# Performance work log

Hardware: AMD Instinct MI355X
Metric: run time of the kernel (lower is better)

Reference implementation:

```python
import jax, jax.numpy as jnp
import numpy as np

BS, L, D = 64, 100, 512
ITEM_NUM = 100000
N = BS * (L + 1)  # number of in-batch candidate items
MASK_VAL = -10000.0


def setup_inputs() -> dict:
    key = jax.random.key(0)
    ks = jax.random.split(key, 8)
    sample_items_id = jax.random.randint(ks[0], (BS, L + 1), 1, ITEM_NUM + 1, dtype=jnp.int32)
    log_mask = jax.random.randint(ks[1], (BS, L), 0, 2, dtype=jnp.int32)
    pop_prob = jax.random.uniform(ks[2], (ITEM_NUM + 1,), minval=1e-3, maxval=1.0, dtype=jnp.float32)
    id_emb = jax.random.normal(ks[3], (ITEM_NUM + 1, D), dtype=jnp.float32) * 0.02
    scale = 1.0 / np.sqrt(D)
    W_ih = jax.random.normal(ks[4], (D, 3 * D), dtype=jnp.float32) * scale
    W_hh = jax.random.normal(ks[5], (D, 3 * D), dtype=jnp.float32) * scale
    b_ih = jnp.zeros((3 * D,), jnp.float32)
    b_hh = jnp.zeros((3 * D,), jnp.float32)
    return dict(sample_items_id=sample_items_id, log_mask=log_mask, pop_prob=pop_prob,
                id_emb=id_emb, W_ih=W_ih, W_hh=W_hh, b_ih=b_ih, b_hh=b_hh)


def gru_forward(x, W_ih, W_hh, b_ih, b_hh):
    # x: (B, T, D) -> per-step hidden states (B, T, D)  (GRU4Rec user encoder)
    B, T, Dh = x.shape
    gates_x = jnp.einsum('btd,de->bte', x, W_ih) + b_ih  # precompute input gates (B,T,3D)

    def step(h, gx):
        gh = h @ W_hh + b_hh
        xr, xz, xn = jnp.split(gx, 3, axis=-1)
        hr, hz, hn = jnp.split(gh, 3, axis=-1)
        r = jax.nn.sigmoid(xr + hr)
        z = jax.nn.sigmoid(xz + hz)
        n = jnp.tanh(xn + r * hn)
        h_new = (1.0 - z) * n + z * h
        return h_new, h_new

    h0 = jnp.zeros((B, Dh), x.dtype)
    _, hs = jax.lax.scan(step, h0, jnp.swapaxes(gates_x, 0, 1))  # (T,B,D)
    return jnp.swapaxes(hs, 0, 1)


def reference(sample_items_id, log_mask, pop_prob, id_emb, W_ih, W_hh, b_ih, b_hh):
    ids_flat = sample_items_id.reshape(-1)                 # (N,)
    debias = jnp.log(pop_prob[ids_flat])                   # (N,) debias_logits
    score_embs = id_emb[ids_flat]                          # (N, D)
    input_embs = score_embs.reshape(BS, L + 1, D)
    prec = gru_forward(input_embs[:, :-1, :], W_ih, W_hh, b_ih, b_hh)  # (BS, L, D)
    prec_vec = prec.reshape(BS * L, D)

    logits = prec_vec @ score_embs.T - debias[None, :]     # (BS*L, N)
    # mask padded candidate columns: cat(log_mask, ones(bs,1)) flattened == 0
    col_valid = jnp.concatenate([log_mask, jnp.ones((BS, 1), log_mask.dtype)], axis=1).reshape(-1)
    logits = jnp.where(col_valid[None, :] == 0, MASK_VAL, logits)
    logits = logits.reshape(BS, L, N)

    # per-sample negative exclusion: column k is rejected for sample i if
    # ids_flat[k] appears anywhere in sample i's own item list
    reject = (ids_flat[None, None, :] == sample_items_id[:, :, None]).any(axis=1)  # (BS, N)
    mask3 = jnp.broadcast_to(reject[:, None, :], (BS, L, N))
    # keep the ground-truth target position (i, j, i*(L+1)+j+1) unmasked
    tgt = jnp.arange(BS)[:, None] * (L + 1) + jnp.arange(L)[None, :] + 1  # (BS, L)
    col = jnp.arange(N)[None, None, :]
    mask3 = mask3 & (col != tgt[:, :, None])
    logits = jnp.where(mask3, MASK_VAL, logits)

    logits = logits.reshape(BS * L, N)
    labels = tgt.reshape(-1)
    logp = jax.nn.log_softmax(logits, axis=-1)
    nll = -jnp.take_along_axis(logp, labels[:, None], axis=1)[:, 0]
    w = (log_mask.reshape(-1) != 0).astype(logits.dtype)
    loss = jnp.sum(nll * w) / jnp.maximum(jnp.sum(w), 1.0)
    return loss
```

## Files before the change

kernel.cpp:

```cpp
#include <hip/hip_runtime.h>
#include <hip/hip_bf16.h>

#define BSZ   64
#define SEQL  100
#define DIM   512
#define L1P   101
#define NCOLS 6464
#define NROWS 6400
#define D3    1536
#define MASKV -10000.0f
#define M0    16.0f

#define SGRP  4
#define SPG   16
#define DBLK  16
#define DPB   32
#define GRU_BLOCKS (SGRP * DBLK)
#define SENT64 0x7FC07FC07FC07FC0ULL
#define INIT_N  409600
#define INIT_NP 410624

typedef __attribute__((ext_vector_type(8))) short bf16x8;
typedef __attribute__((ext_vector_type(4))) float f32x4;

__device__ __forceinline__ float sigm(float x)  { return 1.f / (1.f + __expf(-x)); }
__device__ __forceinline__ float ftanh(float x) { float e = __expf(2.f * x); return 1.f - 2.f / (e + 1.f); }
__device__ __forceinline__ ushort f2bf(float x) {
    __hip_bfloat16 b = __float2bfloat16(x);
    return *(ushort*)&b;
}

__global__ void init_ws(float* s_glob, float* acc, uint4* prec_all)
{
    int t = blockIdx.x * 256 + threadIdx.x;
    if (t < INIT_N) {
        uint4 s; s.x = 0x7FC07FC0u; s.y = 0x7FC07FC0u; s.z = 0x7FC07FC0u; s.w = 0x7FC07FC0u;
        prec_all[t] = s;
    } else if (t < INIT_NP) {
        uint4 z; z.x = 0u; z.y = 0u; z.z = 0u; z.w = 0u;
        prec_all[t] = z;
    }
    if (t < NROWS) s_glob[t] = 0.f;
    if (t < 2) acc[t] = 0.f;
}

__global__ void gather_embs(const int* __restrict__ ids, const float* __restrict__ emb,
                            ushort* __restrict__ score16)
{
    int idx = blockIdx.x * 256 + threadIdx.x;
    int row = idx >> 7, c4 = idx & 127;
    int id = ids[row];
    float4 v = *(const float4*)&emb[(size_t)id * DIM + c4 * 4];
    ushort4 u;
    u.x = f2bf(v.x); u.y = f2bf(v.y); u.z = f2bf(v.z); u.w = f2bf(v.w);
    *(ushort4*)&score16[(size_t)row * DIM + c4 * 4] = u;
}

__global__ void aux_kernel(const int* __restrict__ ids, const float* __restrict__ pop,
                           const int* __restrict__ lmask,
                           float* __restrict__ debias, int* __restrict__ colv)
{
    int k = blockIdx.x * 256 + threadIdx.x;
    if (k >= NCOLS) return;
    int id = ids[k];
    debias[k] = __logf(pop[id]);
    int j = k % L1P;
    colv[k] = (j == SEQL) ? 1 : lmask[(k / L1P) * SEQL + j];
}

__global__ void build_reject(const int* __restrict__ ids, const int* __restrict__ colv,
                             unsigned char* __restrict__ rejm)
{
    __shared__ int s_ids[L1P];
    int i = blockIdx.y;
    int tid = threadIdx.x;
    if (tid < L1P) s_ids[tid] = ids[i * L1P + tid];
    __syncthreads();
    int k = blockIdx.x * 256 + tid;
    if (k >= NCOLS) return;
    int myid = ids[k];
    int rej = 0;
    for (int j = 0; j < L1P; ++j) rej |= (myid == s_ids[j]);
    unsigned char code = (colv[k] == 0) ? 1 : (rej ? 2 : 0);
    rejm[(size_t)i * NCOLS + k] = code;
}

__global__ __launch_bounds__(256) void wt_tile(const float* __restrict__ W,
                                               ushort* __restrict__ WT)
{
    __shared__ float tile[64][65];
    int c0 = blockIdx.x * 64, k0 = blockIdx.y * 64;
    int tx = threadIdx.x & 63, ty = threadIdx.x >> 6;
    for (int r = ty; r < 64; r += 4)
        tile[r][tx] = W[(size_t)(k0 + r) * D3 + c0 + tx];
    __syncthreads();
    for (int r = ty; r < 64; r += 4)
        WT[(size_t)(c0 + r) * DIM + k0 + tx] = f2bf(tile[tx][r]);
}

__global__ __launch_bounds__(256, 1) void gates_mfma(
    const ushort* __restrict__ score16, const ushort* __restrict__ WIT,
    const float* __restrict__ b_ih, float* __restrict__ gates)
{
    __shared__ ushort Bs[64 * 512];
    int n0 = blockIdx.x * 64;
    int rowbase = blockIdx.y * 640;
    int tid = threadIdx.x;
    int w = tid >> 6, lane = tid & 63, l15 = lane & 15, quad = lane >> 4;

    {
        const char* slab = (const char*)(WIT + (size_t)n0 * DIM);
#pragma unroll
        for (int k = 0; k < 16; ++k) {
            int o  = k * 4096 + w * 1024 + lane * 16;
            int so = o ^ (((o >> 10) & 15) << 4);
            __builtin_amdgcn_global_load_lds(
                (const __attribute__((address_space(1))) void*)(slab + so),
                (__attribute__((address_space(3))) void*)((char*)Bs + k * 4096 + w * 1024),
                16, 0, 0);
        }
    }
    float bi[4];
#pragma unroll
    for (int nt = 0; nt < 4; ++nt) bi[nt] = b_ih[n0 + nt * 16 + l15];

    asm volatile("s_waitcnt vmcnt(0)" ::: "memory");
    __syncthreads();

    int key = l15 << 4;
    bf16x8 afA[16], afB[16];

    auto load_af = [&](bf16x8 (&dst)[16], int rt) {
        int r = rowbase + rt * 64 + w * 16 + l15;
        int i = r / SEQL, j = r - i * SEQL;
        const ushort* ap = score16 + (size_t)(i * L1P + j) * DIM + quad * 8;
#pragma unroll
        for (int c = 0; c < 16; ++c) dst[c] = *(const bf16x8*)(ap + c * 32);
    };
    auto do_tile = [&](const bf16x8 (&af)[16], int rt) {
        f32x4 acc[4] = {{0,0,0,0},{0,0,0,0},{0,0,0,0},{0,0,0,0}};
        const char* bt = (const char*)Bs;
#pragma unroll
        for (int c = 0; c < 16; ++c) {
#pragma unroll
            for (int nt = 0; nt < 4; ++nt) {
                int a = (nt * 16 + l15) * 1024 + ((c * 64 + quad * 16) ^ key);
                bf16x8 bb = *(const bf16x8*)(bt + a);
                acc[nt] = __builtin_amdgcn_mfma_f32_16x16x32_bf16(af[c], bb, acc[nt], 0, 0, 0);
            }
        }
#pragma unroll
        for (int nt = 0; nt < 4; ++nt) {
#pragma unroll
            for (int p = 0; p < 4; ++p) {
                int rr = rowbase + rt * 64 + w * 16 + quad * 4 + p;
                gates[(size_t)rr * D3 + n0 + nt * 16 + l15] = acc[nt][p] + bi[nt];
            }
        }
    };

    load_af(afA, 0);
#pragma unroll
    for (int rp = 0; rp < 5; ++rp) {
        load_af(afB, rp * 2 + 1);
        do_tile(afA, rp * 2);
        if (rp < 4) load_af(afA, rp * 2 + 2);
        do_tile(afB, rp * 2 + 1);
    }
}

__global__ __launch_bounds__(256) void gru_mfma(
    const ushort* __restrict__ WT,
    const float* __restrict__ b_hh,
    const float* __restrict__ gates,
    ushort* __restrict__ prec16)
{
    __shared__ float red[2][2][3][256];

    int b = blockIdx.x;
    int sg = b >> 4, db = b & 15;
    int s0 = sg * SPG, d0 = db * DPB;
    int tid = threadIdx.x;
    int w = tid >> 6, lane = tid & 63, l15 = lane & 15, quad = lane >> 4;
    int wc = w & 1, wk = w >> 1;
    int kb = wk * 8;

    bf16x8 wreg[3][8];
#pragma unroll
    for (int g = 0; g < 3; ++g)
#pragma unroll
        for (int cc = 0; cc < 8; ++cc)
            wreg[g][cc] = *(const bf16x8*)(WT
                + (size_t)(g * 512 + d0 + wc * 16 + l15) * DIM
                + (kb + cc) * 32 + quad * 8);

    int d = d0 + wc * 16 + l15;
    float bhr = b_hh[d], bhz = b_hh[512 + d], bhn = b_hh[1024 + d];
    float hprev[4] = {0.f, 0.f, 0.f, 0.f};

    for (int t = 0; t < SEQL; ++t) {
        int tp = t & 1;
        float xr[4], xz[4], xn[4];
        if (wk == 0) {
#pragma unroll
            for (int p = 0; p < 4; ++p) {
                int ss = s0 + quad * 4 + p;
                const float* gx = gates + ((size_t)ss * SEQL + t) * D3;
                xr[p] = gx[d]; xz[p] = gx[512 + d]; xn[p] = gx[1024 + d];
            }
        }
        f32x4 acc[3] = {{0,0,0,0},{0,0,0,0},{0,0,0,0}};
        if (t > 0) {
            const ushort* ap = prec16
                + ((size_t)(s0 + l15) * SEQL + (t - 1)) * DIM + quad * 8;
            unsigned long long v[16];
            bool again = true;
            while (again) {
#pragma unroll
                for (int u = 0; u < 16; ++u) {
                    const unsigned long long* p64 = (const unsigned long long*)
                        (ap + (kb + (u >> 1)) * 32 + (u & 1) * 4);
                    v[u] = __hip_atomic_load(p64, __ATOMIC_RELAXED,
                                             __HIP_MEMORY_SCOPE_AGENT);
                }
                unsigned long long bad = 0ull;
#pragma unroll
                for (int u = 0; u < 16; ++u) {
                    unsigned long long x = v[u] ^ SENT64;
                    bad |= (x - 0x0001000100010001ULL) & ~x & 0x8000800080008000ULL;
                }
                again = (bad != 0ull);
                if (again) __builtin_amdgcn_s_sleep(1);
            }
#pragma unroll
            for (int cc = 0; cc < 8; ++cc) {
                union { unsigned long long q[2]; bf16x8 h; } af;
                af.q[0] = v[2 * cc]; af.q[1] = v[2 * cc + 1];
#pragma unroll
                for (int g = 0; g < 3; ++g)
                    acc[g] = __builtin_amdgcn_mfma_f32_16x16x32_bf16(
                        af.h, wreg[g][cc], acc[g], 0, 0, 0);
            }
        }
        if (wk == 1) {
#pragma unroll
            for (int g = 0; g < 3; ++g)
                *(f32x4*)&red[tp][wc][g][lane * 4] = acc[g];
        }
        __syncthreads();
        if (wk == 0) {
#pragma unroll
            for (int p = 0; p < 4; ++p) {
                float a0 = acc[0][p] + red[tp][wc][0][lane * 4 + p];
                float a1 = acc[1][p] + red[tp][wc][1][lane * 4 + p];
                float a2 = acc[2][p] + red[tp][wc][2][lane * 4 + p];
                float r = sigm(xr[p] + a0 + bhr);
                float z = sigm(xz[p] + a1 + bhz);
                float n = ftanh(xn[p] + r * (a2 + bhn));
                float hnew = (1.f - z) * n + z * hprev[p];
                hprev[p] = hnew;
                unsigned b16 = f2bf(hnew);
                unsigned lo = b16 | (((unsigned)__shfl_xor((int)b16, 1)) << 16);
                unsigned long long hi = (unsigned)__shfl_xor((int)lo, 2);
                unsigned long long vv = (unsigned long long)lo | (hi << 32);
                if ((l15 & 3) == 0) {
                    unsigned long long* dst = (unsigned long long*)
                        (prec16 + ((size_t)(s0 + quad * 4 + p) * SEQL + t) * DIM
                         + d0 + wc * 16 + l15);
                    __hip_atomic_store(dst, vv, __ATOMIC_RELAXED,
                                       __HIP_MEMORY_SCOPE_AGENT);
                }
            }
        }
    }
}

__global__ __launch_bounds__(256, 2) void logits_mfma(
    const ushort* __restrict__ prec16, const ushort* __restrict__ score16,
    const float* __restrict__ debias, const unsigned char* __restrict__ rejm,
    float* __restrict__ s_glob, float* __restrict__ label_glob)
{
    __shared__ ushort Bt[2][16 * 512];
    __shared__ float dbs[816];
    __shared__ unsigned char rjs[816];

    int bi = blockIdx.x;
    int i  = bi >> 3;
    int cs = (bi >> 1) & 3;
    int h  = bi & 1;
    int tile0  = cs * 101 + h * 51;
    int ntiles = 51 - h;
    int tid  = threadIdx.x;
    int lane = tid & 63;
    int w    = tid >> 6;
    int l15  = lane & 15, quad = lane >> 4;

    bf16x8 afrag[2][16];
    bool live1 = (w < 3);
    {
        int r0 = i * SEQL + (2 * w) * 16 + l15;
        const ushort* ap = prec16 + (size_t)r0 * DIM + quad * 8;
#pragma unroll
        for (int c = 0; c < 16; ++c) afrag[0][c] = *(const bf16x8*)(ap + c * 32);
    }
    if (live1) {
        int r1 = i * SEQL + (2 * w + 1) * 16 + l15;
        const ushort* ap = prec16 + (size_t)r1 * DIM + quad * 8;
#pragma unroll
        for (int c = 0; c < 16; ++c) afrag[1][c] = *(const bf16x8*)(ap + c * 32);
    }

    int ncols = ntiles * 16;
    int nb0 = tile0 * 16;
    for (int idx = tid; idx < ncols; idx += 256) {
        dbs[idx] = debias[nb0 + idx];
        rjs[idx] = rejm[(size_t)i * NCOLS + nb0 + idx];
    }

    auto stage = [&](int buf, int st) {
        const char* slab = (const char*)(score16 + (size_t)(tile0 + st) * 16 * DIM);
#pragma unroll
        for (int k = 0; k < 4; ++k) {
            int o  = k * 4096 + w * 1024 + lane * 16;
            int so = o ^ (((o >> 10) & 15) << 4);
            __builtin_amdgcn_global_load_lds(
                (const __attribute__((address_space(1))) void*)(slab + so),
                (__attribute__((address_space(3))) void*)((char*)&Bt[buf][0] + k * 4096 + w * 1024),
                16, 0, 0);
        }
    };

    stage(0, 0);
    asm volatile("s_waitcnt vmcnt(0)" ::: "memory");
    __syncthreads();

    float srun0[4] = {0.f, 0.f, 0.f, 0.f};
    float srun1[4] = {0.f, 0.f, 0.f, 0.f};
    int colb = l15 * 1024;
    int q16  = quad * 16;
    int key  = l15 << 4;

    for (int st = 0; st < ntiles; ++st) {
        int cur = st & 1;
        if (st + 1 < ntiles) stage(cur ^ 1, st + 1);

        const char* bt = (const char*)&Bt[cur][0];
        f32x4 acc0[2] = {{0,0,0,0},{0,0,0,0}};
        f32x4 acc1[2] = {{0,0,0,0},{0,0,0,0}};
#pragma unroll
        for (int c = 0; c < 16; ++c) {
            int a = colb + ((c * 64 + q16) ^ key);
            bf16x8 b = *(const bf16x8*)(bt + a);
            acc0[c & 1] = __builtin_amdgcn_mfma_f32_16x16x32_bf16(afrag[0][c], b, acc0[c & 1], 0, 0, 0);
            if (live1)
                acc1[c & 1] = __builtin_amdgcn_mfma_f32_16x16x32_bf16(afrag[1][c], b, acc1[c & 1], 0, 0, 0);
        }

        int mi = st * 16 + l15;
        int n  = nb0 + mi;
        float db = dbs[mi];
        int   mc = rjs[mi];
        int   jj = n - i * L1P - 1;
        {
            int rowb = (2 * w) * 16 + quad * 4;
#pragma unroll
            for (int p = 0; p < 4; ++p) {
                int j = rowb + p;
                float l = acc0[0][p] + acc0[1][p] - db;
                bool is_t = (j == jj);
                bool msk = (mc == 1) || (mc == 2 && !is_t);
                l = msk ? MASKV : l;
                if (is_t && j < SEQL) label_glob[i * SEQL + j] = l;
                if (j < SEQL) srun0[p] += __expf(l - M0);
            }
        }
        if (live1) {
            int rowb = (2 * w + 1) * 16 + quad * 4;
#pragma unroll
            for (int p = 0; p < 4; ++p) {
                int j = rowb + p;
                float l = acc1[0][p] + acc1[1][p] - db;
                bool is_t = (j == jj);
                bool msk = (mc == 1) || (mc == 2 && !is_t);
                l = msk ? MASKV : l;
                if (is_t && j < SEQL) label_glob[i * SEQL + j] = l;
                if (j < SEQL) srun1[p] += __expf(l - M0);
            }
        }
        __syncthreads();
    }

#pragma unroll
    for (int p = 0; p < 4; ++p) {
        float s = srun0[p];
        s += __shfl_xor(s, 1); s += __shfl_xor(s, 2);
        s += __shfl_xor(s, 4); s += __shfl_xor(s, 8);
        if (l15 == 0) {
            int j = (2 * w) * 16 + quad * 4 + p;
            if (j < SEQL) atomicAdd(&s_glob[i * SEQL + j], s);
        }
    }
    if (live1) {
#pragma unroll
        for (int p = 0; p < 4; ++p) {
            float s = srun1[p];
            s += __shfl_xor(s, 1); s += __shfl_xor(s, 2);
            s += __shfl_xor(s, 4); s += __shfl_xor(s, 8);
            if (l15 == 0) {
                int j = (2 * w + 1) * 16 + quad * 4 + p;
                if (j < SEQL) atomicAdd(&s_glob[i * SEQL + j], s);
            }
        }
    }
}

__global__ void nll_reduce(const float* __restrict__ s_glob, const float* __restrict__ label_glob,
                           const int* __restrict__ lmask, float* __restrict__ acc)
{
    int r = blockIdx.x * 256 + threadIdx.x;
    float v = 0.f, wt = 0.f;
    if (r < NROWS) {
        wt = (lmask[r] != 0) ? 1.f : 0.f;
        v  = (M0 + __logf(s_glob[r]) - label_glob[r]) * wt;
    }
#pragma unroll
    for (int o = 32; o; o >>= 1) { v += __shfl_down(v, o); wt += __shfl_down(wt, o); }
    if ((threadIdx.x & 63) == 0) { atomicAdd(&acc[0], v); atomicAdd(&acc[1], wt); }
}

__global__ void finalize(const float* __restrict__ acc, float* __restrict__ out)
{
    out[0] = acc[0] / fmaxf(acc[1], 1.f);
}

extern "C" void kernel_launch(void* const* d_in, const int* in_sizes, int n_in,
                              void* d_out, int out_size, void* d_ws, size_t ws_size,
                              hipStream_t stream)
{
    const int*   ids   = (const int*)d_in[0];
    const int*   lmask = (const int*)d_in[1];
    const float* pop   = (const float*)d_in[2];
    const float* emb   = (const float*)d_in[3];
    const float* W_ih  = (const float*)d_in[4];
    const float* W_hh  = (const float*)d_in[5];
    const float* b_ih  = (const float*)d_in[6];
    const float* b_hh  = (const float*)d_in[7];
    float* out = (float*)d_out;

    ushort* score16 = (ushort*)d_ws;
    ushort* prec16  = score16 + (size_t)NCOLS * DIM;
    ushort* WT      = prec16 + (size_t)(NROWS + 16) * DIM;
    ushort* WIT     = WT + (size_t)D3 * DIM;
    float*  debias  = (float*)(WIT + (size_t)D3 * DIM);
    int*    colv    = (int*)(debias + NCOLS);
    unsigned char* rejm = (unsigned char*)(colv + NCOLS);
    float*  gates   = (float*)(rejm + (size_t)BSZ * NCOLS + 64);
    float*  s_glob  = gates + (size_t)NROWS * D3;
    float*  label_g = s_glob + NROWS;
    float*  acc     = label_g + NROWS;

    init_ws<<<INIT_NP / 256, 256, 0, stream>>>(s_glob, acc, (uint4*)prec16);
    gather_embs<<<(NCOLS * 128) / 256, 256, 0, stream>>>(ids, emb, score16);
    aux_kernel<<<(NCOLS + 255) / 256, 256, 0, stream>>>(ids, pop, lmask, debias, colv);
    build_reject<<<dim3((NCOLS + 255) / 256, BSZ), 256, 0, stream>>>(ids, colv, rejm);
    wt_tile<<<dim3(24, 8), 256, 0, stream>>>(W_hh, WT);
    wt_tile<<<dim3(24, 8), 256, 0, stream>>>(W_ih, WIT);
    gates_mfma<<<dim3(24, 10), 256, 0, stream>>>(score16, WIT, b_ih, gates);
    gru_mfma<<<GRU_BLOCKS, 256, 0, stream>>>(WT, b_hh, gates, prec16);
    logits_mfma<<<BSZ * 8, 256, 0, stream>>>(prec16, score16, debias, rejm, s_glob, label_g);
    nll_reduce<<<(NROWS + 255) / 256, 256, 0, stream>>>(s_glob, label_g, lmask, acc);
    finalize<<<1, 1, 0, stream>>>(acc, out);
}
```

Baseline: 911.6 us.

## Fuse prologue kernels into one launch and stage GRU hidden-state publish through LDS

Merges the six setup kernels (workspace init, embedding gather, debias, reject-mask build, two weight transposes) into one block-partitioned prologue kernel. The separate colv buffer goes away because column validity is now computed inline. In the GRU recurrence, new hidden values are staged in shared memory, and a second warp group publishes them as packed 64-bit atomic stores, replacing the per-lane shuffles. This costs an extra __syncthreads per step, and the reduction buffer is no longer double-buffered. The goal is to cut launch overhead and shorten the serial per-step publish path.

```diff
diff --git a/kernel.cpp b/kernel.cpp
--- a/kernel.cpp
+++ b/kernel.cpp
@@ -20,6 +20,18 @@
 #define INIT_N  409600
 #define INIT_NP 410624
 
+#define PB_GATHER0 0
+#define PB_GATHERN 3232
+#define PB_REJ0    (PB_GATHER0 + PB_GATHERN)
+#define PB_REJN    1664
+#define PB_INIT0   (PB_REJ0 + PB_REJN)
+#define PB_INITN   1604
+#define PB_WT0     (PB_INIT0 + PB_INITN)
+#define PB_WTN     384
+#define PB_AUX0    (PB_WT0 + PB_WTN)
+#define PB_AUXN    26
+#define PB_TOTAL   (PB_AUX0 + PB_AUXN)
+
 typedef __attribute__((ext_vector_type(8))) short bf16x8;
 typedef __attribute__((ext_vector_type(4))) float f32x4;
 
@@ -30,72 +42,71 @@
     return *(ushort*)&b;
 }
 
-__global__ void init_ws(float* s_glob, float* acc, uint4* prec_all)
-{
-    int t = blockIdx.x * 256 + threadIdx.x;
-    if (t < INIT_N) {
-        uint4 s; s.x = 0x7FC07FC0u; s.y = 0x7FC07FC0u; s.z = 0x7FC07FC0u; s.w = 0x7FC07FC0u;
-        prec_all[t] = s;
-    } else if (t < INIT_NP) {
-        uint4 z; z.x = 0u; z.y = 0u; z.z = 0u; z.w = 0u;
-        prec_all[t] = z;
-    }
-    if (t < NROWS) s_glob[t] = 0.f;
-    if (t < 2) acc[t] = 0.f;
-}
-
-__global__ void gather_embs(const int* __restrict__ ids, const float* __restrict__ emb,
-                            ushort* __restrict__ score16)
-{
-    int idx = blockIdx.x * 256 + threadIdx.x;
-    int row = idx >> 7, c4 = idx & 127;
-    int id = ids[row];
-    float4 v = *(const float4*)&emb[(size_t)id * DIM + c4 * 4];
-    ushort4 u;
-    u.x = f2bf(v.x); u.y = f2bf(v.y); u.z = f2bf(v.z); u.w = f2bf(v.w);
-    *(ushort4*)&score16[(size_t)row * DIM + c4 * 4] = u;
-}
-
-__global__ void aux_kernel(const int* __restrict__ ids, const float* __restrict__ pop,
-                           const int* __restrict__ lmask,
-                           float* __restrict__ debias, int* __restrict__ colv)
-{
-    int k = blockIdx.x * 256 + threadIdx.x;
-    if (k >= NCOLS) return;
-    int id = ids[k];
-    debias[k] = __logf(pop[id]);
-    int j = k % L1P;
-    colv[k] = (j == SEQL) ? 1 : lmask[(k / L1P) * SEQL + j];
-}
-
-__global__ void build_reject(const int* __restrict__ ids, const int* __restrict__ colv,
-                             unsigned char* __restrict__ rejm)
-{
-    __shared__ int s_ids[L1P];
-    int i = blockIdx.y;
+__global__ __launch_bounds__(256) void prologue(
+    const int* __restrict__ ids, const int* __restrict__ lmask,
+    const float* __restrict__ pop, const float* __restrict__ emb,
+    const float* __restrict__ W_hh, const float* __restrict__ W_ih,
+    ushort* __restrict__ score16, uint4* __restrict__ prec_all,
+    ushort* __restrict__ WT, ushort* __restrict__ WIT,
+    float* __restrict__ debias, unsigned char* __restrict__ rejm,
+    float* __restrict__ s_glob, float* __restrict__ acc)
+{
+    __shared__ union {
+        float tile[64][65];
+        int   s_ids[L1P];
+    } sm;
+    int bid = blockIdx.x;
     int tid = threadIdx.x;
-    if (tid < L1P) s_ids[tid] = ids[i * L1P + tid];
-    __syncthreads();
-    int k = blockIdx.x * 256 + tid;
-    if (k >= NCOLS) return;
-    int myid = ids[k];
-    int rej = 0;
-    for (int j = 0; j < L1P; ++j) rej |= (myid == s_ids[j]);
-    unsigned char code = (colv[k] == 0) ? 1 : (rej ? 2 : 0);
-    rejm[(size_t)i * NCOLS + k] = code;
-}
-
-__global__ __launch_bounds__(256) void wt_tile(const float* __restrict__ W,
-                                               ushort* __restrict__ WT)
-{
-    __shared__ float tile[64][65];
-    int c0 = blockIdx.x * 64, k0 = blockIdx.y * 64;
-    int tx = threadIdx.x & 63, ty = threadIdx.x >> 6;
-    for (int r = ty; r < 64; r += 4)
-        tile[r][tx] = W[(size_t)(k0 + r) * D3 + c0 + tx];
-    __syncthreads();
-    for (int r = ty; r < 64; r += 4)
-        WT[(size_t)(c0 + r) * DIM + k0 + tx] = f2bf(tile[tx][r]);
+
+    if (bid < PB_REJ0) {
+        int idx = bid * 256 + tid;
+        int row = idx >> 7, c4 = idx & 127;
+        int id = ids[row];
+        float4 v = *(const float4*)&emb[(size_t)id * DIM + c4 * 4];
+        ushort4 u;
+        u.x = f2bf(v.x); u.y = f2bf(v.y); u.z = f2bf(v.z); u.w = f2bf(v.w);
+        *(ushort4*)&score16[(size_t)row * DIM + c4 * 4] = u;
+    } else if (bid < PB_INIT0) {
+        int rb = bid - PB_REJ0;
+        int i  = rb / 26, kb = rb % 26;
+        if (tid < L1P) sm.s_ids[tid] = ids[i * L1P + tid];
+        __syncthreads();
+        int k = kb * 256 + tid;
+        if (k >= NCOLS) return;
+        int myid = ids[k];
+        int rej = 0;
+        for (int j = 0; j < L1P; ++j) rej |= (myid == sm.s_ids[j]);
+        int j = k % L1P;
+        int cv = (j == SEQL) ? 1 : lmask[(k / L1P) * SEQL + j];
+        rejm[(size_t)i * NCOLS + k] = (cv == 0) ? 1 : (rej ? 2 : 0);
+    } else if (bid < PB_WT0) {
+        int t = (bid - PB_INIT0) * 256 + tid;
+        if (t < INIT_N) {
+            uint4 s; s.x = 0x7FC07FC0u; s.y = 0x7FC07FC0u; s.z = 0x7FC07FC0u; s.w = 0x7FC07FC0u;
+            prec_all[t] = s;
+        } else {
+            uint4 z; z.x = 0u; z.y = 0u; z.z = 0u; z.w = 0u;
+            prec_all[t] = z;
+        }
+        if (t < NROWS) s_glob[t] = 0.f;
+        if (t < 2) acc[t] = 0.f;
+    } else if (bid < PB_AUX0) {
+        int wb = bid - PB_WT0;
+        int which = wb / 192, r = wb % 192;
+        const float* W = which ? W_ih : W_hh;
+        ushort* WTd    = which ? WIT  : WT;
+        int c0 = (r % 24) * 64, k0 = (r / 24) * 64;
+        int tx = tid & 63, ty = tid >> 6;
+        for (int rr = ty; rr < 64; rr += 4)
+            sm.tile[rr][tx] = W[(size_t)(k0 + rr) * D3 + c0 + tx];
+        __syncthreads();
+        for (int rr = ty; rr < 64; rr += 4)
+            WTd[(size_t)(c0 + rr) * DIM + k0 + tx] = f2bf(sm.tile[tx][rr]);
+    } else {
+        int k = (bid - PB_AUX0) * 256 + tid;
+        if (k >= NCOLS) return;
+        debias[k] = __logf(pop[ids[k]]);
+    }
 }
 
 __global__ __launch_bounds__(256, 1) void gates_mfma(
@@ -175,7 +186,8 @@
     const float* __restrict__ gates,
     ushort* __restrict__ prec16)
 {
-    __shared__ float red[2][2][3][256];
+    __shared__ float  red[2][3][256];
+    __shared__ ushort hpub[16][32];
 
     int b = blockIdx.x;
     int sg = b >> 4, db = b & 15;
@@ -199,7 +211,6 @@
     float hprev[4] = {0.f, 0.f, 0.f, 0.f};
 
     for (int t = 0; t < SEQL; ++t) {
-        int tp = t & 1;
         float xr[4], xz[4], xn[4];
         if (wk == 0) {
 #pragma unroll
@@ -245,32 +256,36 @@
         if (wk == 1) {
 #pragma unroll
             for (int g = 0; g < 3; ++g)
-                *(f32x4*)&red[tp][wc][g][lane * 4] = acc[g];
+                *(f32x4*)&red[wc][g][lane * 4] = acc[g];
         }
         __syncthreads();
         if (wk == 0) {
 #pragma unroll
             for (int p = 0; p < 4; ++p) {
-                float a0 = acc[0][p] + red[tp][wc][0][lane * 4 + p];
-                float a1 = acc[1][p] + red[tp][wc][1][lane * 4 + p];
-                float a2 = acc[2][p] + red[tp][wc][2][lane * 4 + p];
+                float a0 = acc[0][p] + red[wc][0][lane * 4 + p];
+                float a1 = acc[1][p] + red[wc][1][lane * 4 + p];
+                float a2 = acc[2][p] + red[wc][2][lane * 4 + p];
                 float r = sigm(xr[p] + a0 + bhr);
                 float z = sigm(xz[p] + a1 + bhz);
                 float n = ftanh(xn[p] + r * (a2 + bhn));
                 float hnew = (1.f - z) * n + z * hprev[p];
                 hprev[p] = hnew;
-                unsigned b16 = f2bf(hnew);
-                unsigned lo = b16 | (((unsigned)__shfl_xor((int)b16, 1)) << 16);
-                unsigned long long hi = (unsigned)__shfl_xor((int)lo, 2);
-                unsigned long long vv = (unsigned long long)lo | (hi << 32);
-                if ((l15 & 3) == 0) {
-                    unsigned long long* dst = (unsigned long long*)
-                        (prec16 + ((size_t)(s0 + quad * 4 + p) * SEQL + t) * DIM
-                         + d0 + wc * 16 + l15);
-                    __hip_atomic_store(dst, vv, __ATOMIC_RELAXED,
-                                       __HIP_MEMORY_SCOPE_AGENT);
-                }
-            }
+                hpub[quad * 4 + p][wc * 16 + l15] = f2bf(hnew);
+            }
+        }
+        __syncthreads();
+        if (tid >= 128) {
+            int pt = tid - 128;
+            int ss = pt >> 3, gq = pt & 7;
+            unsigned long long vv =
+                 (unsigned long long)hpub[ss][gq * 4 + 0]
+               | ((unsigned long long)hpub[ss][gq * 4 + 1] << 16)
+               | ((unsigned long long)hpub[ss][gq * 4 + 2] << 32)
+               | ((unsigned long long)hpub[ss][gq * 4 + 3] << 48);
+            unsigned long long* dst = (unsigned long long*)
+                (prec16 + ((size_t)(s0 + ss) * SEQL + t) * DIM + d0 + gq * 4);
+            __hip_atomic_store(dst, vv, __ATOMIC_RELAXED,
+                               __HIP_MEMORY_SCOPE_AGENT);
         }
     }
 }
@@ -452,19 +467,15 @@
     ushort* WT      = prec16 + (size_t)(NROWS + 16) * DIM;
     ushort* WIT     = WT + (size_t)D3 * DIM;
     float*  debias  = (float*)(WIT + (size_t)D3 * DIM);
-    int*    colv    = (int*)(debias + NCOLS);
-    unsigned char* rejm = (unsigned char*)(colv + NCOLS);
+    unsigned char* rejm = (unsigned char*)(debias + NCOLS);
     float*  gates   = (float*)(rejm + (size_t)BSZ * NCOLS + 64);
     float*  s_glob  = gates + (size_t)NROWS * D3;
     float*  label_g = s_glob + NROWS;
     float*  acc     = label_g + NROWS;
 
-    init_ws<<<INIT_NP / 256, 256, 0, stream>>>(s_glob, acc, (uint4*)prec16);
-    gather_embs<<<(NCOLS * 128) / 256, 256, 0, stream>>>(ids, emb, score16);
-    aux_kernel<<<(NCOLS + 255) / 256, 256, 0, stream>>>(ids, pop, lmask, debias, colv);
-    build_reject<<<dim3((NCOLS + 255) / 256, BSZ), 256, 0, stream>>>(ids, colv, rejm);
-    wt_tile<<<dim3(24, 8), 256, 0, stream>>>(W_hh, WT);
-    wt_tile<<<dim3(24, 8), 256, 0, stream>>>(W_ih, WIT);
+    prologue<<<PB_TOTAL, 256, 0, stream>>>(ids, lmask, pop, emb, W_hh, W_ih,
+                                           score16, (uint4*)prec16, WT, WIT,
+                                           debias, rejm, s_glob, acc);
     gates_mfma<<<dim3(24, 10), 256, 0, stream>>>(score16, WIT, b_ih, gates);
     gru_mfma<<<GRU_BLOCKS, 256, 0, stream>>>(WT, b_hh, gates, prec16);
     logits_mfma<<<BSZ * 8, 256, 0, stream>>>(prec16, score16, debias, rejm, s_glob, label_g);
```

Measured after the change: 773.1 us. 1.18x faster.
